# Kernel optimization log

Hardware: AMD Instinct MI355X
Metric: run time of the kernel (lower is better)

The kernel has to match this reference:

```python
import jax, jax.numpy as jnp
import numpy as np

B, S, D, H, BLK, R = 2, 4096, 768, 12, 64, 3
NB = S // BLK  # 64 blocks
HD = D // H    # 64 head dim


def layer_norm(x, g, b, eps=1e-6):
    m = jnp.mean(x, -1, keepdims=True)
    v = jnp.mean((x - m) ** 2, -1, keepdims=True)
    return (x - m) / jnp.sqrt(v + eps) * g + b


def bigbird_attention(x, wq, bq, wk, bk, wv, bv, wo, bo, rand_attn):
    # x: [B,S,D]; rand_attn: [H, NB-2, R] int block indices
    def heads(t):
        return t.reshape(B, S, H, HD).transpose(0, 2, 1, 3)  # [B,H,S,HD]
    q = heads(x @ wq + bq)
    k = heads(x @ wk + bk)
    v = heads(x @ wv + bv)
    scale = 1.0 / jnp.sqrt(jnp.asarray(HD, x.dtype))

    qb = q.reshape(B, H, NB, BLK, HD)
    kb = k.reshape(B, H, NB, BLK, HD)
    vb = v.reshape(B, H, NB, BLK, HD)

    # --- global query blocks (first & last) attend to the full sequence ---
    qg = jnp.concatenate([qb[:, :, :1], qb[:, :, -1:]], axis=2)  # [B,H,2,BLK,HD]
    sg = jnp.einsum('bhnqd,bhkd->bhnqk', qg, k) * scale          # [B,H,2,BLK,S]
    og = jnp.einsum('bhnqk,bhkd->bhnqd', jax.nn.softmax(sg, -1), v)

    # --- middle query blocks: global(2) + window(3) + random(R) key blocks ---
    mids = jnp.arange(1, NB - 1)                                  # [NB-2]
    win = jnp.stack([mids - 1, mids, mids + 1], -1)               # [NB-2,3]
    glb = jnp.broadcast_to(jnp.array([0, NB - 1]), (NB - 2, 2))   # [NB-2,2]
    fixed = jnp.concatenate([glb, win], -1)                       # [NB-2,5]
    idx = jnp.concatenate(
        [jnp.broadcast_to(fixed, (H, NB - 2, 5)), rand_attn], -1)  # [H,NB-2,5+R]
    h_ix = jnp.arange(H)[:, None, None]
    km = kb[:, h_ix, idx].reshape(B, H, NB - 2, (5 + R) * BLK, HD)
    vm = vb[:, h_ix, idx].reshape(B, H, NB - 2, (5 + R) * BLK, HD)
    sm = jnp.einsum('bhnqd,bhnkd->bhnqk', qb[:, :, 1:-1], km) * scale
    om = jnp.einsum('bhnqk,bhnkd->bhnqd', jax.nn.softmax(sm, -1), vm)

    ob = jnp.concatenate([og[:, :, :1], om, og[:, :, 1:]], axis=2)  # [B,H,NB,BLK,HD]
    out = ob.reshape(B, H, S, HD).transpose(0, 2, 1, 3).reshape(B, S, D)
    return out @ wo + bo


def mlp(x, w1, b1, w2, b2):
    return jax.nn.gelu(x @ w1 + b1) @ w2 + b2


def setup_inputs() -> dict:
    key = jax.random.key(0)
    ks = jax.random.split(key, 8)
    s = 0.02
    return {
        'x': jax.random.normal(ks[0], (B, S, D, 2), jnp.float32),
        'ln1_g': jnp.ones((D,), jnp.float32),
        'ln1_b': jnp.zeros((D,), jnp.float32),
        'ln2_g': jnp.ones((D,), jnp.float32),
        'ln2_b': jnp.zeros((D,), jnp.float32),
        'wq': jax.random.normal(ks[1], (D, D), jnp.float32) * s,
        'bq': jnp.zeros((D,), jnp.float32),
        'wk': jax.random.normal(ks[2], (D, D), jnp.float32) * s,
        'bk': jnp.zeros((D,), jnp.float32),
        'wv': jax.random.normal(ks[3], (D, D), jnp.float32) * s,
        'bv': jnp.zeros((D,), jnp.float32),
        'wo': jax.random.normal(ks[4], (D, D), jnp.float32) * s,
        'bo': jnp.zeros((D,), jnp.float32),
        'w1': jax.random.normal(ks[5], (D, 4 * D), jnp.float32) * s,
        'b1': jnp.zeros((4 * D,), jnp.float32),
        'w2': jax.random.normal(ks[6], (4 * D, D), jnp.float32) * s,
        'b2': jnp.zeros((D,), jnp.float32),
        'rand_attn': jax.random.randint(ks[7], (H, NB - 2, R), 1, NB - 1),
    }


def reference(x, ln1_g, ln1_b, ln2_g, ln2_b, wq, bq, wk, bk, wv, bv, wo, bo,
              w1, b1, w2, b2, rand_attn):
    # x: [B,S,D,2]; chunk(2,-1): first chunk -> x2, second -> x1
    x2 = x[..., 0]
    x1 = x[..., 1]
    y2 = x2 + bigbird_attention(layer_norm(x1, ln1_g, ln1_b),
                                wq, bq, wk, bk, wv, bv, wo, bo, rand_attn)
    y1 = x1 + mlp(layer_norm(y2, ln2_g, ln2_b), w1, b1, w2, b2)
    return jnp.stack([y1, y2], axis=-1)  # cat([y1,y2], -1)
```

## Files before the change

kernel.cpp:

```cpp
#include <hip/hip_runtime.h>
#include <cstdint>
#include <cstddef>

typedef __attribute__((ext_vector_type(8))) short bfr8;
typedef __attribute__((ext_vector_type(4))) float acc4;

__device__ __forceinline__ float bf2f(short s) {
  return __uint_as_float(((unsigned)(unsigned short)s) << 16);
}
__device__ __forceinline__ short f2bf(float f) {
  unsigned u = __float_as_uint(f);
  u += 0x7fffu + ((u >> 16) & 1u);
  return (short)(u >> 16);
}
__device__ __forceinline__ float gelu_f(float x) {
  float z = 0.7978845608028654f * (x + 0.044715f * x * x * x);
  z = fminf(fmaxf(z, -12.f), 12.f);
  float e = __expf(2.f * z);
  float th = (e - 1.f) / (e + 1.f);
  return 0.5f * x * (1.f + th);
}
__device__ __forceinline__ void load_lds16(const short* g, short* l) {
  __builtin_amdgcn_global_load_lds(
      (const __attribute__((address_space(1))) void*)g,
      (__attribute__((address_space(3))) void*)l, 16, 0, 0);
}

#define BB 2
#define SS 4096
#define DD 768
#define HH 12
#define BLKSZ 64
#define NBLK 64
#define HDIM 64

__global__ __launch_bounds__(256) void prep_weights(
    const float* __restrict__ wq, const float* __restrict__ wk,
    const float* __restrict__ wv, const float* __restrict__ wo,
    const float* __restrict__ w1, const float* __restrict__ w2,
    const float* __restrict__ bq, const float* __restrict__ bk,
    const float* __restrict__ bv, float* __restrict__ bqkv,
    short* __restrict__ wqT, short* __restrict__ wkT, short* __restrict__ wvT,
    short* __restrict__ woT, short* __restrict__ w1T, short* __restrict__ w2T) {
  int id = blockIdx.x;
  if (id >= 6912) {
    int t = (id - 6912) * 256 + threadIdx.x;
    bqkv[t] = (t < 768) ? bq[t] : (t < 1536) ? bk[t - 768] : bv[t - 1536];
    return;
  }
  const float* src; short* dst; int K, N, n0, k0;
  if (id < 2304) {
    int seg = id / 576, local = id % 576;
    K = 768; N = 768;
    n0 = (local % 24) * 32; k0 = (local / 24) * 32;
    src = seg == 0 ? wq : seg == 1 ? wk : seg == 2 ? wv : wo;
    dst = seg == 0 ? wqT : seg == 1 ? wkT : seg == 2 ? wvT : woT;
  } else if (id < 4608) {
    int local = id - 2304;
    K = 768; N = 3072;
    n0 = (local % 96) * 32; k0 = (local / 96) * 32;
    src = w1; dst = w1T;
  } else {
    int local = id - 4608;
    K = 3072; N = 768;
    n0 = (local % 24) * 32; k0 = (local / 24) * 32;
    src = w2; dst = w2T;
  }
  __shared__ float tile[32][33];
  int tx = threadIdx.x & 31, ty = threadIdx.x >> 5;
#pragma unroll
  for (int i = 0; i < 4; i++) {
    int kk = ty + i * 8;
    tile[kk][tx] = src[(size_t)(k0 + kk) * N + n0 + tx];
  }
  __syncthreads();
#pragma unroll
  for (int i = 0; i < 4; i++) {
    int nn = ty + i * 8;
    dst[(size_t)(n0 + nn) * K + k0 + tx] = f2bf(tile[tx][nn]);
  }
}

__global__ __launch_bounds__(256) void transpose_bf16(
    const short* __restrict__ src, short* __restrict__ dst) {
  __shared__ short tile[32][33];
  int b = blockIdx.z;
  int s0 = blockIdx.x * 32, d0 = blockIdx.y * 32;
  int tx = threadIdx.x & 31, ty = threadIdx.x >> 5;
#pragma unroll
  for (int i = 0; i < 4; i++) {
    int ss = ty + i * 8;
    tile[ss][tx] = src[((size_t)b * SS + s0 + ss) * DD + d0 + tx];
  }
  __syncthreads();
#pragma unroll
  for (int i = 0; i < 4; i++) {
    int dd = ty + i * 8;
    dst[((size_t)b * DD + d0 + dd) * SS + s0 + tx] = tile[tx][dd];
  }
}

__global__ __launch_bounds__(256) void ln_kernel(
    const float* __restrict__ in, int stride, int off,
    const float* __restrict__ gam, const float* __restrict__ bet,
    short* __restrict__ out) {
  int row = blockIdx.x;
  int t = threadIdx.x;
  const float* base = in + (size_t)row * 768 * stride + off;
  float vals[3], s = 0.f, s2 = 0.f;
#pragma unroll
  for (int i = 0; i < 3; i++) {
    int d = t + 256 * i;
    float v = base[(size_t)d * stride];
    vals[i] = v; s += v; s2 += v * v;
  }
#pragma unroll
  for (int o = 32; o; o >>= 1) { s += __shfl_down(s, o); s2 += __shfl_down(s2, o); }
  __shared__ float red[8];
  int lane = t & 63, w = t >> 6;
  if (lane == 0) { red[w] = s; red[4 + w] = s2; }
  __syncthreads();
  s = red[0] + red[1] + red[2] + red[3];
  s2 = red[4] + red[5] + red[6] + red[7];
  float mean = s * (1.f / 768.f);
  float var = s2 * (1.f / 768.f) - mean * mean;
  float rstd = rsqrtf(var + 1e-6f);
#pragma unroll
  for (int i = 0; i < 3; i++) {
    int d = t + 256 * i;
    out[(size_t)row * 768 + d] = f2bf((vals[i] - mean) * rstd * gam[d] + bet[d]);
  }
}

template <int BM, int BN, int EPI, int SWZ>
__global__ __launch_bounds__(256) void gemm_lds(
    const short* __restrict__ A, const short* __restrict__ BT,
    const float* __restrict__ bias, const float* __restrict__ xres,
    const float* __restrict__ aux, void* __restrict__ outp, int M, int N, int K) {
  __shared__ alignas(16) short As[2][BM * 64];
  __shared__ alignas(16) short Bs[2][BN * 64];
  constexpr int TI = BM / 32;
  constexpr int TJ = BN / 32;
  static_assert(TI + TJ == 8, "vmcnt(8) immediate assumes 8 loads/tile/wave");
  int orig = blockIdx.x + gridDim.x * blockIdx.y;
  int gx = gridDim.x;
  int mchunk = gridDim.y >> 3;
  int xcd = orig & 7, l = orig >> 3;
  int mb, nb;
  if (SWZ == 0) { nb = l / mchunk; mb = xcd * mchunk + (l % mchunk); }
  else          { nb = l % gx;     mb = xcd * mchunk + (l / gx); }
  int m0 = mb * BM, n0 = nb * BN;
  int t = threadIdx.x;
  int lane = t & 63, wave = t >> 6;
  int wm = (wave >> 1) * (BM / 2), wn = (wave & 1) * (BN / 2);
  int quad = lane >> 4, lc = lane & 15;
  acc4 acc[TI][TJ];
#pragma unroll
  for (int i = 0; i < TI; i++)
#pragma unroll
    for (int j = 0; j < TJ; j++) acc[i][j] = (acc4){0.f, 0.f, 0.f, 0.f};

  int lrow = lane >> 3;
  int scol = ((lane & 7) ^ lrow) * 8;
  const short* Ag = A + (size_t)(m0 + wave * (BM / 4) + lrow) * K + scol;
  const short* Bg = BT + (size_t)(n0 + wave * (BN / 4) + lrow) * K + scol;
  int aoff = wave * (BM * 16);
  int boff = wave * (BN * 16);
  int rsw = (lc & 7) << 4;

  const int nk = K >> 6;
#pragma unroll
  for (int j = 0; j < TI; j++)
    load_lds16(Ag + (size_t)(j * 8) * K, &As[0][aoff + j * 512]);
#pragma unroll
  for (int j = 0; j < TJ; j++)
    load_lds16(Bg + (size_t)(j * 8) * K, &Bs[0][boff + j * 512]);
  if (nk > 1) {
#pragma unroll
    for (int j = 0; j < TI; j++)
      load_lds16(Ag + 64 + (size_t)(j * 8) * K, &As[1][aoff + j * 512]);
#pragma unroll
    for (int j = 0; j < TJ; j++)
      load_lds16(Bg + 64 + (size_t)(j * 8) * K, &Bs[1][boff + j * 512]);
  }

  for (int it = 0; it < nk; ++it) {
    int cur = it & 1;
    if (it + 1 < nk) asm volatile("s_waitcnt vmcnt(8)" ::: "memory");
    else             asm volatile("s_waitcnt vmcnt(0)" ::: "memory");
    __builtin_amdgcn_s_barrier();
    __builtin_amdgcn_sched_barrier(0);
    const char* Ab = (const char*)&As[cur][0];
    const char* Bb = (const char*)&Bs[cur][0];
#pragma unroll
    for (int kk = 0; kk < 2; kk++) {
      int rboff = ((kk << 6) | (quad << 4)) ^ rsw;
      bfr8 afr[TI], bfr[TJ];
#pragma unroll
      for (int i = 0; i < TI; i++)
        afr[i] = *(const bfr8*)(Ab + (wm + i * 16 + lc) * 128 + rboff);
#pragma unroll
      for (int j = 0; j < TJ; j++)
        bfr[j] = *(const bfr8*)(Bb + (wn + j * 16 + lc) * 128 + rboff);
#pragma unroll
      for (int i = 0; i < TI; i++)
#pragma unroll
        for (int j = 0; j < TJ; j++)
          acc[i][j] = __builtin_amdgcn_mfma_f32_16x16x32_bf16(afr[i], bfr[j], acc[i][j], 0, 0, 0);
    }
    if (it < nk - 2) {
      __builtin_amdgcn_sched_barrier(0);
      __builtin_amdgcn_s_barrier();
      __builtin_amdgcn_sched_barrier(0);
      int k0 = (it + 2) << 6;
#pragma unroll
      for (int j = 0; j < TI; j++)
        load_lds16(Ag + k0 + (size_t)(j * 8) * K, &As[cur][aoff + j * 512]);
#pragma unroll
      for (int j = 0; j < TJ; j++)
        load_lds16(Bg + k0 + (size_t)(j * 8) * K, &Bs[cur][boff + j * 512]);
    }
  }
#pragma unroll
  for (int i = 0; i < TI; i++) {
#pragma unroll
    for (int j = 0; j < TJ; j++) {
      int col = n0 + wn + j * 16 + lc;
      float bv = bias[col];
#pragma unroll
      for (int r = 0; r < 4; r++) {
        int row = m0 + wm + i * 16 + quad * 4 + r;
        float v = acc[i][j][r] + bv;
        size_t idx = (size_t)row * N + col;
        if (EPI == 1) {
          v += xres[idx * 2];
          ((float*)outp)[idx * 2 + 1] = v;
        } else if (EPI == 2) {
          ((short*)outp)[idx] = f2bf(gelu_f(v));
        } else if (EPI == 3) {
          v += xres[idx * 2 + 1];
          ((float*)outp)[idx * 2] = v;
        } else if (EPI == 4) {
          int bufidx = col / 768;
          int colm = col - bufidx * 768;
          ((short*)outp)[(size_t)bufidx * 6291456 + (size_t)row * 768 + colm] = f2bf(v);
        } else if (EPI == 5) {
          v += xres[idx * 2];
          ((float*)outp)[idx] = v;
        } else {
          v += xres[idx * 2 + 1];
          float2 pr; pr.x = v; pr.y = aux[idx];
          ((float2*)outp)[idx] = pr;
        }
      }
    }
  }
}

__device__ __forceinline__ void attn_core(
    const short* __restrict__ qrow0, const short* __restrict__ kbase,
    const short* __restrict__ vt_h, const int* kblist, int nch, int t,
    short (*QPs)[72], short (*Ks)[72], short (*Vts)[72],
    float* m, float* l, acc4* O) {
  int lane = t & 63, w = t >> 6, quad = lane >> 4, lc = lane & 15;
#pragma unroll
  for (int c = t; c < 512; c += 256) {
    int r = c >> 3, dc = c & 7;
    *(bfr8*)&QPs[r][dc * 8] = *(const bfr8*)&qrow0[(size_t)r * DD + dc * 8];
  }
  __syncthreads();
  bfr8 aq0 = *(const bfr8*)&QPs[w * 16 + lc][quad * 8];
  bfr8 aq1 = *(const bfr8*)&QPs[w * 16 + lc][32 + quad * 8];
#pragma unroll
  for (int r = 0; r < 4; r++) { m[r] = -1e30f; l[r] = 0.f; }
#pragma unroll
  for (int dt = 0; dt < 4; dt++) O[dt] = (acc4){0.f, 0.f, 0.f, 0.f};

  for (int ch = 0; ch < nch; ch++) {
    int kb = kblist[ch];
    __syncthreads();
#pragma unroll
    for (int c = t; c < 512; c += 256) {
      int r = c >> 3, dc = c & 7;
      *(bfr8*)&Ks[r][dc * 8] = *(const bfr8*)&kbase[((size_t)kb * 64 + r) * DD + dc * 8];
      *(bfr8*)&Vts[r][dc * 8] = *(const bfr8*)&vt_h[(size_t)r * SS + kb * 64 + dc * 8];
    }
    __syncthreads();
    acc4 sacc[4];
#pragma unroll
    for (int nt = 0; nt < 4; nt++) {
      bfr8 bk0 = *(const bfr8*)&Ks[nt * 16 + lc][quad * 8];
      bfr8 bk1 = *(const bfr8*)&Ks[nt * 16 + lc][32 + quad * 8];
      acc4 z = (acc4){0.f, 0.f, 0.f, 0.f};
      z = __builtin_amdgcn_mfma_f32_16x16x32_bf16(aq0, bk0, z, 0, 0, 0);
      z = __builtin_amdgcn_mfma_f32_16x16x32_bf16(aq1, bk1, z, 0, 0, 0);
      sacc[nt] = z;
    }
#pragma unroll
    for (int r = 0; r < 4; r++) {
      float sv[4];
#pragma unroll
      for (int nt = 0; nt < 4; nt++) sv[nt] = sacc[nt][r] * 0.125f;
      float cm = fmaxf(fmaxf(sv[0], sv[1]), fmaxf(sv[2], sv[3]));
      cm = fmaxf(cm, __shfl_xor(cm, 1));
      cm = fmaxf(cm, __shfl_xor(cm, 2));
      cm = fmaxf(cm, __shfl_xor(cm, 4));
      cm = fmaxf(cm, __shfl_xor(cm, 8));
      float mn = fmaxf(m[r], cm);
      float al = __expf(m[r] - mn);
      m[r] = mn;
      float ls = 0.f;
#pragma unroll
      for (int nt = 0; nt < 4; nt++) {
        float p = __expf(sv[nt] - mn);
        ls += p;
        QPs[w * 16 + quad * 4 + r][nt * 16 + lc] = f2bf(p);
      }
      ls += __shfl_xor(ls, 1);
      ls += __shfl_xor(ls, 2);
      ls += __shfl_xor(ls, 4);
      ls += __shfl_xor(ls, 8);
      l[r] = l[r] * al + ls;
#pragma unroll
      for (int dt = 0; dt < 4; dt++) O[dt][r] *= al;
    }
    bfr8 ap0 = *(const bfr8*)&QPs[w * 16 + lc][quad * 8];
    bfr8 ap1 = *(const bfr8*)&QPs[w * 16 + lc][32 + quad * 8];
#pragma unroll
    for (int dt = 0; dt < 4; dt++) {
      bfr8 bv0 = *(const bfr8*)&Vts[dt * 16 + lc][quad * 8];
      bfr8 bv1 = *(const bfr8*)&Vts[dt * 16 + lc][32 + quad * 8];
      O[dt] = __builtin_amdgcn_mfma_f32_16x16x32_bf16(ap0, bv0, O[dt], 0, 0, 0);
      O[dt] = __builtin_amdgcn_mfma_f32_16x16x32_bf16(ap1, bv1, O[dt], 0, 0, 0);
    }
  }
}

__global__ __launch_bounds__(256) void attn_mid_mfma(
    const short* __restrict__ qbuf, const short* __restrict__ kbuf,
    const short* __restrict__ vtbuf, const int* __restrict__ rand_attn,
    short* __restrict__ ao) {
  int n = 1 + blockIdx.x;
  int h = blockIdx.y, b = blockIdx.z;
  int t = threadIdx.x, lane = t & 63, w = t >> 6, quad = lane >> 4, lc = lane & 15;
  int hoff = h * HDIM;
  size_t btok = (size_t)b * SS;
  __shared__ alignas(16) short QPs[64][72], Ks[64][72], Vts[64][72];
  int kblist[8];
  kblist[0] = 0; kblist[1] = NBLK - 1;
  kblist[2] = n - 1; kblist[3] = n; kblist[4] = n + 1;
#pragma unroll
  for (int r = 0; r < 3; r++)
    kblist[5 + r] = rand_attn[((size_t)h * 62 + (n - 1)) * 3 + r];
  float m[4], l[4]; acc4 O[4];
  attn_core(qbuf + (btok + (size_t)n * 64) * DD + hoff,
            kbuf + btok * DD + hoff,
            vtbuf + ((size_t)b * DD + hoff) * SS,
            kblist, 8, t, QPs, Ks, Vts, m, l, O);
#pragma unroll
  for (int r = 0; r < 4; r++) {
    float inv = 1.f / l[r];
    size_t tok = btok + (size_t)n * 64 + w * 16 + quad * 4 + r;
    short* op = ao + tok * DD + hoff;
#pragma unroll
    for (int dt = 0; dt < 4; dt++) op[dt * 16 + lc] = f2bf(O[dt][r] * inv);
  }
}

__global__ __launch_bounds__(256) void attn_glb_mfma(
    const short* __restrict__ qbuf, const short* __restrict__ kbuf,
    const short* __restrict__ vtbuf, float* __restrict__ part) {
  int g = blockIdx.x & 1, s = blockIdx.x >> 1;
  int h = blockIdx.y, b = blockIdx.z;
  int t = threadIdx.x, lane = t & 63, w = t >> 6, quad = lane >> 4, lc = lane & 15;
  int hoff = h * HDIM;
  size_t btok = (size_t)b * SS;
  int qblk = g ? (NBLK - 1) : 0;
  __shared__ alignas(16) short QPs[64][72], Ks[64][72], Vts[64][72];
  int kblist[8];
#pragma unroll
  for (int c = 0; c < 8; c++) kblist[c] = s * 8 + c;
  float m[4], l[4]; acc4 O[4];
  attn_core(qbuf + (btok + (size_t)qblk * 64) * DD + hoff,
            kbuf + btok * DD + hoff,
            vtbuf + ((size_t)b * DD + hoff) * SS,
            kblist, 8, t, QPs, Ks, Vts, m, l, O);
  float* pp = part + ((((size_t)b * HH + h) * 2 + g) * 8 + s) * 4224;
#pragma unroll
  for (int r = 0; r < 4; r++) {
    int row = w * 16 + quad * 4 + r;
#pragma unroll
    for (int dt = 0; dt < 4; dt++) pp[row * 64 + dt * 16 + lc] = O[dt][r];
    if (lc == 0) {
      pp[4096 + row] = m[r];
      pp[4160 + row] = l[r];
    }
  }
}

__global__ __launch_bounds__(256) void attn_combine(
    const float* __restrict__ part, short* __restrict__ ao) {
  int g = blockIdx.x, h = blockIdx.y, b = blockIdx.z;
  int t = threadIdx.x, qrow = t >> 2, sub = t & 3;
  const float* base = part + (((size_t)b * HH + h) * 2 + g) * 8 * 4224;
  float mm[8], ll[8], M = -1e30f;
#pragma unroll
  for (int s = 0; s < 8; s++) {
    mm[s] = base[s * 4224 + 4096 + qrow];
    ll[s] = base[s * 4224 + 4160 + qrow];
    M = fmaxf(M, mm[s]);
  }
  float L = 0.f, O[16];
#pragma unroll
  for (int d = 0; d < 16; d++) O[d] = 0.f;
#pragma unroll
  for (int s = 0; s < 8; s++) {
    float w = __expf(mm[s] - M);
    L += w * ll[s];
    const float* Op = base + s * 4224 + qrow * 64 + sub * 16;
#pragma unroll
    for (int d = 0; d < 16; d++) O[d] += w * Op[d];
  }
  float inv = 1.f / L;
  int qblk = g ? (NBLK - 1) : 0;
  size_t tok = (size_t)b * SS + (size_t)qblk * BLKSZ + qrow;
  short* op = ao + tok * DD + h * HDIM + sub * 16;
#pragma unroll
  for (int d = 0; d < 16; d++) op[d] = f2bf(O[d] * inv);
}

extern "C" void kernel_launch(void* const* d_in, const int* in_sizes, int n_in,
                              void* d_out, int out_size, void* d_ws, size_t ws_size,
                              hipStream_t stream) {
  (void)in_sizes; (void)n_in; (void)out_size;
  const float* x     = (const float*)d_in[0];
  const float* ln1_g = (const float*)d_in[1];
  const float* ln1_b = (const float*)d_in[2];
  const float* ln2_g = (const float*)d_in[3];
  const float* ln2_b = (const float*)d_in[4];
  const float* wq = (const float*)d_in[5];
  const float* bq = (const float*)d_in[6];
  const float* wk = (const float*)d_in[7];
  const float* bk = (const float*)d_in[8];
  const float* wv = (const float*)d_in[9];
  const float* bv = (const float*)d_in[10];
  const float* wo = (const float*)d_in[11];
  const float* bo = (const float*)d_in[12];
  const float* w1 = (const float*)d_in[13];
  const float* b1 = (const float*)d_in[14];
  const float* w2 = (const float*)d_in[15];
  const float* b2 = (const float*)d_in[16];
  const int* rand_attn = (const int*)d_in[17];
  float* out = (float*)d_out;

  short* wsb = (short*)d_ws;
  const size_t WD = 589824;
  const size_t WB = 2359296;
  const size_t ACT = 6291456;
  short* wqT = wsb;
  short* wkT = wqT + WD;
  short* wvT = wkT + WD;
  short* woT = wvT + WD;
  short* w1T = woT + WD;
  short* w2T = w1T + WB;
  short* xln = w2T + WB;
  short* qb  = xln + ACT;
  short* kb  = qb + ACT;
  short* vb  = kb + ACT;
  short* aob = vb + ACT;
  float* partp = (float*)(aob + ACT);
  float* bqkv = partp + 1622016;
  float* y2f  = bqkv + 2304;
  short* vbT = xln;
  short* h1 = xln;
  short* ln2b = aob;

  const size_t NEED = ((size_t)(y2f + ACT) - (size_t)d_ws);
  bool big = ws_size >= NEED;

  prep_weights<<<6921, 256, 0, stream>>>(wq, wk, wv, wo, w1, w2, bq, bk, bv, bqkv,
                                         wqT, wkT, wvT, woT, w1T, w2T);

  ln_kernel<<<8192, 256, 0, stream>>>(x, 2, 1, ln1_g, ln1_b, xln);

  gemm_lds<128, 128, 4, 0><<<dim3(18, 64), 256, 0, stream>>>(
      xln, wqT, bqkv, nullptr, nullptr, qb, 8192, 2304, 768);

  transpose_bf16<<<dim3(128, 24, 2), 256, 0, stream>>>(vb, vbT);

  attn_mid_mfma<<<dim3(62, 12, 2), 256, 0, stream>>>(qb, kb, vbT, rand_attn, aob);
  attn_glb_mfma<<<dim3(16, 12, 2), 256, 0, stream>>>(qb, kb, vbT, partp);
  attn_combine<<<dim3(2, 12, 2), 256, 0, stream>>>(partp, aob);

  if (big) {
    gemm_lds<128, 128, 5, 0><<<dim3(6, 64), 256, 0, stream>>>(
        aob, woT, bo, x, nullptr, y2f, 8192, 768, 768);
    ln_kernel<<<8192, 256, 0, stream>>>(y2f, 1, 0, ln2_g, ln2_b, ln2b);
    gemm_lds<128, 128, 2, 0><<<dim3(24, 64), 256, 0, stream>>>(
        ln2b, w1T, b1, nullptr, nullptr, h1, 8192, 3072, 768);
    gemm_lds<128, 128, 6, 1><<<dim3(6, 64), 256, 0, stream>>>(
        h1, w2T, b2, x, y2f, out, 8192, 768, 3072);
  } else {
    gemm_lds<128, 128, 1, 0><<<dim3(6, 64), 256, 0, stream>>>(
        aob, woT, bo, x, nullptr, out, 8192, 768, 768);
    ln_kernel<<<8192, 256, 0, stream>>>((const float*)d_out, 2, 1, ln2_g, ln2_b, ln2b);
    gemm_lds<128, 128, 2, 0><<<dim3(24, 64), 256, 0, stream>>>(
        ln2b, w1T, b1, nullptr, nullptr, h1, 8192, 3072, 768);
    gemm_lds<128, 128, 3, 1><<<dim3(6, 64), 256, 0, stream>>>(
        h1, w2T, b2, x, nullptr, out, 8192, 768, 3072);
  }
}
```

Before: 436.0 us.

## Add 256x256 eight-phase pipelined MFMA GEMM for QKV and MLP-up projections

Introduces a new 512-thread GEMM kernel with 256x256 tiles that interleaves async global-to-LDS loads with MFMA phases, using double buffers, setprio and explicit vmcnt waits. The bf16 epilogue is staged through LDS so stores are coalesced. The kernel replaces the 128x128 GEMM for the QKV projection and the MLP first layer. The aim is more operand reuse per tile and better overlap of memory traffic with matrix math. The cost is 128KB of dynamic LDS and heavy register use, and the small grids (288 and 384 blocks) may leave some CUs underused.

```diff
diff --git a/kernel.cpp b/kernel.cpp
--- a/kernel.cpp
+++ b/kernel.cpp
@@ -4,6 +4,7 @@
 
 typedef __attribute__((ext_vector_type(8))) short bfr8;
 typedef __attribute__((ext_vector_type(4))) float acc4;
+typedef __attribute__((ext_vector_type(4))) float f32x4;
 
 __device__ __forceinline__ float bf2f(short s) {
   return __uint_as_float(((unsigned)(unsigned short)s) << 16);
@@ -257,6 +258,179 @@
   }
 }
 
+template <int BN, int EPI, int SWZ>
+__global__ __launch_bounds__(512, 2) void gemm_8ph(
+    const short* __restrict__ A, const short* __restrict__ BT,
+    const float* __restrict__ bias, const float* __restrict__ xres,
+    const float* __restrict__ aux, void* __restrict__ outp, int M, int N, int K) {
+  constexpr int NJ = BN / 64;
+  constexpr int NJ2 = NJ / 2;
+  constexpr int LB = BN / 128;
+  extern __shared__ short lds[];
+  int gx = gridDim.x;
+  int orig = blockIdx.x + gx * blockIdx.y;
+  int mchunk = gridDim.y >> 3;
+  int xcd = orig & 7, l = orig >> 3;
+  int mb, nb;
+  if (SWZ == 0) { nb = l / mchunk; mb = xcd * mchunk + (l % mchunk); }
+  else          { nb = l % gx;     mb = xcd * mchunk + (l / gx); }
+  int m0 = mb * 256, n0 = nb * BN;
+  const int t = threadIdx.x;
+  const int lane = t & 63, wave = t >> 6;
+  const int wm = (wave >> 2) * 128;
+  const int wn = (wave & 3) * (BN / 4);
+  const int quad = lane >> 4, lc = lane & 15;
+  const int rsw = (lc & 7) << 4;
+
+  const int srow = t >> 3;
+  const int sg = ((t & 7) ^ (srow & 7)) * 8;
+  const short* Asrc = A + (size_t)(m0 + srow) * K + sg;
+  const short* Bsrc = BT + (size_t)(n0 + srow) * K + sg;
+
+  acc4 acc[8][NJ];
+#pragma unroll
+  for (int i = 0; i < 8; i++)
+#pragma unroll
+    for (int j = 0; j < NJ; j++) acc[i][j] = (acc4){0.f, 0.f, 0.f, 0.f};
+  bfr8 a0[4][2], a1[4][2], b0[NJ2][2], b1[NJ2][2];
+
+#define SA_(buf, half, c, kt) load_lds16(Asrc + ((size_t)((half)*128 + (c)*64)) * K + (size_t)(kt) * 64, \
+                                         lds + (buf)*16384 + ((half)*128 + (c)*64)*64 + t*8)
+#define SB_(buf, half, c, kt) load_lds16(Bsrc + ((size_t)((half)*(BN/2) + (c)*64)) * K + (size_t)(kt) * 64, \
+                                         lds + 32768 + (buf)*(BN*64) + ((half)*(BN/2) + (c)*64)*64 + t*8)
+#define SAH(buf, half, kt) do { SA_(buf, half, 0, kt); SA_(buf, half, 1, kt); } while (0)
+#define SBH(buf, half, kt) do { SB_(buf, half, 0, kt); if (LB == 2) SB_(buf, half, 1, kt); } while (0)
+#define RA_(arr, buf, half) \
+  _Pragma("unroll") for (int i_ = 0; i_ < 4; i_++) \
+  _Pragma("unroll") for (int k_ = 0; k_ < 2; k_++) \
+    arr[i_][k_] = *(const bfr8*)((const char*)lds + (buf)*32768 + \
+        (wm + (half)*64 + i_*16 + lc)*128 + (((k_<<6)|(quad<<4)) ^ rsw))
+#define RB_(arr, buf, half) \
+  _Pragma("unroll") for (int j_ = 0; j_ < NJ2; j_++) \
+  _Pragma("unroll") for (int k_ = 0; k_ < 2; k_++) \
+    arr[j_][k_] = *(const bfr8*)((const char*)lds + 65536 + (buf)*(BN*128) + \
+        (wn + (half)*(NJ2*16) + j_*16 + lc)*128 + (((k_<<6)|(quad<<4)) ^ rsw))
+#define MM_(aarr, barr, i0, j0) \
+  _Pragma("unroll") for (int i_ = 0; i_ < 4; i_++) \
+  _Pragma("unroll") for (int j_ = 0; j_ < NJ2; j_++) \
+  _Pragma("unroll") for (int k_ = 0; k_ < 2; k_++) \
+    acc[(i0)+i_][(j0)+j_] = __builtin_amdgcn_mfma_f32_16x16x32_bf16( \
+        aarr[i_][k_], barr[j_][k_], acc[(i0)+i_][(j0)+j_], 0, 0, 0)
+#define P1_ __builtin_amdgcn_s_setprio(1)
+#define P0_ __builtin_amdgcn_s_setprio(0)
+#define FENCE_BAR do { __builtin_amdgcn_sched_barrier(0); __builtin_amdgcn_s_barrier(); } while (0)
+#define VM_CNT do { if constexpr (LB == 2) asm volatile("s_waitcnt vmcnt(4)" ::: "memory"); \
+                    else                   asm volatile("s_waitcnt vmcnt(3)" ::: "memory"); } while (0)
+#define VM_ZERO asm volatile("s_waitcnt vmcnt(0)" ::: "memory")
+
+  const int nk = K >> 6;
+  SAH(0, 0, 0); SAH(0, 1, 0); SBH(0, 0, 0); SBH(0, 1, 0);
+  SBH(1, 0, 1); SAH(1, 0, 1);
+  VM_CNT;
+  FENCE_BAR;
+
+  for (int it = 0; it < nk; it += 2) {
+    const bool more = (it + 2) < nk;
+    RA_(a0, 0, 0); RB_(b0, 0, 0); SAH(1, 1, it + 1);
+    P1_; MM_(a0, b0, 0, 0); P0_; FENCE_BAR;
+    RB_(b1, 0, 1); SBH(1, 1, it + 1);
+    P1_; MM_(a0, b1, 0, NJ2); P0_; FENCE_BAR;
+    RA_(a1, 0, 1); if (more) SBH(0, 0, it + 2);
+    P1_; MM_(a1, b0, 4, 0); P0_; FENCE_BAR;
+    if (more) SAH(0, 0, it + 2);
+    P1_; MM_(a1, b1, 4, NJ2); P0_;
+    if (more) { VM_CNT; } else { VM_ZERO; }
+    FENCE_BAR;
+    RA_(a0, 1, 0); RB_(b0, 1, 0); if (more) SAH(0, 1, it + 2);
+    P1_; MM_(a0, b0, 0, 0); P0_; FENCE_BAR;
+    RB_(b1, 1, 1); if (more) SBH(0, 1, it + 2);
+    P1_; MM_(a0, b1, 0, NJ2); P0_; FENCE_BAR;
+    RA_(a1, 1, 1); if (more) SBH(1, 0, it + 3);
+    P1_; MM_(a1, b0, 4, 0); P0_; FENCE_BAR;
+    if (more) SAH(1, 0, it + 3);
+    P1_; MM_(a1, b1, 4, NJ2); P0_;
+    if (more) { VM_CNT; }
+    FENCE_BAR;
+  }
+#undef SA_
+#undef SB_
+#undef SAH
+#undef SBH
+#undef RA_
+#undef RB_
+#undef MM_
+#undef P1_
+#undef P0_
+#undef FENCE_BAR
+#undef VM_CNT
+#undef VM_ZERO
+
+  if constexpr (EPI == 2 || EPI == 4) {
+    short* ot = lds;
+#pragma unroll
+    for (int i = 0; i < 8; i++)
+#pragma unroll
+      for (int j = 0; j < NJ; j++) {
+        int col = wn + j * 16 + lc;
+        float bv = bias[n0 + col];
+#pragma unroll
+        for (int r = 0; r < 4; r++) {
+          int row = wm + i * 16 + quad * 4 + r;
+          float v = acc[i][j][r] + bv;
+          if (EPI == 2) v = gelu_f(v);
+          ot[row * BN + col] = f2bf(v);
+        }
+      }
+    __syncthreads();
+    constexpr int CPR = BN / 8;
+    short* obase; int ostride;
+    if (EPI == 4) {
+      int bufidx = n0 / 768;
+      obase = (short*)outp + (size_t)bufidx * 6291456 + (size_t)m0 * 768 + (n0 - bufidx * 768);
+      ostride = 768;
+    } else {
+      obase = (short*)outp + (size_t)m0 * N + n0;
+      ostride = N;
+    }
+#pragma unroll
+    for (int q = 0; q < 256 * CPR / 512; q++) {
+      int c = q * 512 + t;
+      int row = c / CPR, ch = c % CPR;
+      *(f32x4*)(obase + (size_t)row * ostride + ch * 8) =
+          *(const f32x4*)(ot + row * BN + ch * 8);
+    }
+  } else {
+#pragma unroll
+    for (int i = 0; i < 8; i++) {
+#pragma unroll
+      for (int j = 0; j < NJ; j++) {
+        int col = n0 + wn + j * 16 + lc;
+        float bv = bias[col];
+#pragma unroll
+        for (int r = 0; r < 4; r++) {
+          int row = m0 + wm + i * 16 + quad * 4 + r;
+          float v = acc[i][j][r] + bv;
+          size_t idx = (size_t)row * N + col;
+          if (EPI == 1) {
+            v += xres[idx * 2];
+            ((float*)outp)[idx * 2 + 1] = v;
+          } else if (EPI == 3) {
+            v += xres[idx * 2 + 1];
+            ((float*)outp)[idx * 2] = v;
+          } else if (EPI == 5) {
+            v += xres[idx * 2];
+            ((float*)outp)[idx] = v;
+          } else {
+            v += xres[idx * 2 + 1];
+            float2 pr; pr.x = v; pr.y = aux[idx];
+            ((float2*)outp)[idx] = pr;
+          }
+        }
+      }
+    }
+  }
+}
+
 __device__ __forceinline__ void attn_core(
     const short* __restrict__ qrow0, const short* __restrict__ kbase,
     const short* __restrict__ vt_h, const int* kblist, int nch, int t,
@@ -478,12 +652,14 @@
   const size_t NEED = ((size_t)(y2f + ACT) - (size_t)d_ws);
   bool big = ws_size >= NEED;
 
+  const size_t LDS_256 = 131072;
+
   prep_weights<<<6921, 256, 0, stream>>>(wq, wk, wv, wo, w1, w2, bq, bk, bv, bqkv,
                                          wqT, wkT, wvT, woT, w1T, w2T);
 
   ln_kernel<<<8192, 256, 0, stream>>>(x, 2, 1, ln1_g, ln1_b, xln);
 
-  gemm_lds<128, 128, 4, 0><<<dim3(18, 64), 256, 0, stream>>>(
+  gemm_8ph<256, 4, 0><<<dim3(9, 32), 512, LDS_256, stream>>>(
       xln, wqT, bqkv, nullptr, nullptr, qb, 8192, 2304, 768);
 
   transpose_bf16<<<dim3(128, 24, 2), 256, 0, stream>>>(vb, vbT);
@@ -496,7 +672,7 @@
     gemm_lds<128, 128, 5, 0><<<dim3(6, 64), 256, 0, stream>>>(
         aob, woT, bo, x, nullptr, y2f, 8192, 768, 768);
     ln_kernel<<<8192, 256, 0, stream>>>(y2f, 1, 0, ln2_g, ln2_b, ln2b);
-    gemm_lds<128, 128, 2, 0><<<dim3(24, 64), 256, 0, stream>>>(
+    gemm_8ph<256, 2, 0><<<dim3(12, 32), 512, LDS_256, stream>>>(
         ln2b, w1T, b1, nullptr, nullptr, h1, 8192, 3072, 768);
     gemm_lds<128, 128, 6, 1><<<dim3(6, 64), 256, 0, stream>>>(
         h1, w2T, b2, x, y2f, out, 8192, 768, 3072);
```

Result: slower. 451.4 us (+3.5%).

## Double-buffer K/V tiles in attention with register prefetch of next chunk

Applied to the files above, without the earlier changes.

The shared attention core now keeps two LDS buffers for the K and V-transposed tiles. Each iteration loads the next key block into registers before the MFMA and softmax work on the current block, then stores it into the other buffer afterwards. This hides global-load latency behind compute and drops one barrier per chunk. The cost is more LDS per block (two K/V buffers), which may lower occupancy, plus extra registers held across the compute.

```diff
diff --git a/kernel.cpp b/kernel.cpp
--- a/kernel.cpp
+++ b/kernel.cpp
@@ -260,13 +260,20 @@
 __device__ __forceinline__ void attn_core(
     const short* __restrict__ qrow0, const short* __restrict__ kbase,
     const short* __restrict__ vt_h, const int* kblist, int nch, int t,
-    short (*QPs)[72], short (*Ks)[72], short (*Vts)[72],
+    short (*QPs)[72], short (*Ksb)[64][72], short (*Vtsb)[64][72],
     float* m, float* l, acc4* O) {
   int lane = t & 63, w = t >> 6, quad = lane >> 4, lc = lane & 15;
-#pragma unroll
-  for (int c = t; c < 512; c += 256) {
-    int r = c >> 3, dc = c & 7;
-    *(bfr8*)&QPs[r][dc * 8] = *(const bfr8*)&qrow0[(size_t)r * DD + dc * 8];
+  const int ra = t >> 3;
+  const int rb = ra + 32;
+  const int ca = (t & 7) * 8;
+  *(bfr8*)&QPs[ra][ca] = *(const bfr8*)&qrow0[(size_t)ra * DD + ca];
+  *(bfr8*)&QPs[rb][ca] = *(const bfr8*)&qrow0[(size_t)rb * DD + ca];
+  {
+    int kb = kblist[0];
+    *(bfr8*)&Ksb[0][ra][ca] = *(const bfr8*)&kbase[((size_t)kb * 64 + ra) * DD + ca];
+    *(bfr8*)&Ksb[0][rb][ca] = *(const bfr8*)&kbase[((size_t)kb * 64 + rb) * DD + ca];
+    *(bfr8*)&Vtsb[0][ra][ca] = *(const bfr8*)&vt_h[(size_t)ra * SS + kb * 64 + ca];
+    *(bfr8*)&Vtsb[0][rb][ca] = *(const bfr8*)&vt_h[(size_t)rb * SS + kb * 64 + ca];
   }
   __syncthreads();
   bfr8 aq0 = *(const bfr8*)&QPs[w * 16 + lc][quad * 8];
@@ -277,15 +284,18 @@
   for (int dt = 0; dt < 4; dt++) O[dt] = (acc4){0.f, 0.f, 0.f, 0.f};
 
   for (int ch = 0; ch < nch; ch++) {
-    int kb = kblist[ch];
-    __syncthreads();
-#pragma unroll
-    for (int c = t; c < 512; c += 256) {
-      int r = c >> 3, dc = c & 7;
-      *(bfr8*)&Ks[r][dc * 8] = *(const bfr8*)&kbase[((size_t)kb * 64 + r) * DD + dc * 8];
-      *(bfr8*)&Vts[r][dc * 8] = *(const bfr8*)&vt_h[(size_t)r * SS + kb * 64 + dc * 8];
-    }
-    __syncthreads();
+    int cur = ch & 1;
+    short (*Ks)[72] = Ksb[cur];
+    short (*Vts)[72] = Vtsb[cur];
+    bfr8 kA, kB, vA, vB;
+    const bool pf = (ch + 1 < nch);
+    if (pf) {
+      int kb = kblist[ch + 1];
+      kA = *(const bfr8*)&kbase[((size_t)kb * 64 + ra) * DD + ca];
+      kB = *(const bfr8*)&kbase[((size_t)kb * 64 + rb) * DD + ca];
+      vA = *(const bfr8*)&vt_h[(size_t)ra * SS + kb * 64 + ca];
+      vB = *(const bfr8*)&vt_h[(size_t)rb * SS + kb * 64 + ca];
+    }
     acc4 sacc[4];
 #pragma unroll
     for (int nt = 0; nt < 4; nt++) {
@@ -333,6 +343,14 @@
       O[dt] = __builtin_amdgcn_mfma_f32_16x16x32_bf16(ap0, bv0, O[dt], 0, 0, 0);
       O[dt] = __builtin_amdgcn_mfma_f32_16x16x32_bf16(ap1, bv1, O[dt], 0, 0, 0);
     }
+    if (pf) {
+      int nxt = cur ^ 1;
+      *(bfr8*)&Ksb[nxt][ra][ca] = kA;
+      *(bfr8*)&Ksb[nxt][rb][ca] = kB;
+      *(bfr8*)&Vtsb[nxt][ra][ca] = vA;
+      *(bfr8*)&Vtsb[nxt][rb][ca] = vB;
+    }
+    __syncthreads();
   }
 }
 
@@ -345,7 +363,8 @@
   int t = threadIdx.x, lane = t & 63, w = t >> 6, quad = lane >> 4, lc = lane & 15;
   int hoff = h * HDIM;
   size_t btok = (size_t)b * SS;
-  __shared__ alignas(16) short QPs[64][72], Ks[64][72], Vts[64][72];
+  __shared__ alignas(16) short QPs[64][72];
+  __shared__ alignas(16) short Ksb[2][64][72], Vtsb[2][64][72];
   int kblist[8];
   kblist[0] = 0; kblist[1] = NBLK - 1;
   kblist[2] = n - 1; kblist[3] = n; kblist[4] = n + 1;
@@ -356,7 +375,7 @@
   attn_core(qbuf + (btok + (size_t)n * 64) * DD + hoff,
             kbuf + btok * DD + hoff,
             vtbuf + ((size_t)b * DD + hoff) * SS,
-            kblist, 8, t, QPs, Ks, Vts, m, l, O);
+            kblist, 8, t, QPs, Ksb, Vtsb, m, l, O);
 #pragma unroll
   for (int r = 0; r < 4; r++) {
     float inv = 1.f / l[r];
@@ -376,7 +395,8 @@
   int hoff = h * HDIM;
   size_t btok = (size_t)b * SS;
   int qblk = g ? (NBLK - 1) : 0;
-  __shared__ alignas(16) short QPs[64][72], Ks[64][72], Vts[64][72];
+  __shared__ alignas(16) short QPs[64][72];
+  __shared__ alignas(16) short Ksb[2][64][72], Vtsb[2][64][72];
   int kblist[8];
 #pragma unroll
   for (int c = 0; c < 8; c++) kblist[c] = s * 8 + c;
@@ -384,7 +404,7 @@
   attn_core(qbuf + (btok + (size_t)qblk * 64) * DD + hoff,
             kbuf + btok * DD + hoff,
             vtbuf + ((size_t)b * DD + hoff) * SS,
-            kblist, 8, t, QPs, Ks, Vts, m, l, O);
+            kblist, 8, t, QPs, Ksb, Vtsb, m, l, O);
   float* pp = part + ((((size_t)b * HH + h) * 2 + g) * 8 + s) * 4224;
 #pragma unroll
   for (int r = 0; r < 4; r++) {
```

Measured after the change: 437.0 us. Within noise of the previous version (+0.2%).
